# Performance work log

Measured on AMD Instinct MI355X. Metric: run time of the kernel, lower is better.

Reference implementation:

```python
import jax, jax.numpy as jnp
import numpy as np


def setup_inputs() -> dict:
    key = jax.random.key(0)
    k1, k2, k3, k4 = jax.random.split(key, 4)
    B, S, K, N = 4, 2048, 4096, 4096
    # int8-valued quantized activations / weights (held in int32 containers)
    a = jax.random.randint(k1, (B, S, K), -128, 128, dtype=jnp.int32)
    w = jax.random.randint(k2, (K, N), -128, 128, dtype=jnp.int32)
    # per-token activation scale and per-output-column weight scale
    a_scale = jax.random.uniform(k3, (B, S, 1), dtype=jnp.float32) * 0.01
    w_scale = jax.random.uniform(k4, (1, N), dtype=jnp.float32) * 0.01
    return {"a": a, "a_scale": a_scale, "w": w, "w_scale": w_scale}


def reference(a, a_scale, w, w_scale):
    # int8 GEMM with int32 accumulation (torch._int_mm equivalent),
    # batched over B instead of a per-slice Python loop.
    acc = jnp.einsum("bsk,kn->bsn", a, w)  # int32 accumulate
    # dequant epilogue: out = acc * (a_scale * w_scale), then cast to model dtype
    out = acc.astype(jnp.float32) * (a_scale * w_scale)  # [B,S,N]
    return out.astype(jnp.float32)
```

## Files before the change

### kernel.cpp

```cpp
#include <hip/hip_runtime.h>


#define M_TOT 8192
#define N_TOT 4096
#define K_TOT 4096
#define NT_K  (K_TOT / 64)
#define TILE_BYTES 16384

typedef int v4i  __attribute__((ext_vector_type(4)));
typedef int v16i __attribute__((ext_vector_type(16)));

typedef const __attribute__((address_space(1))) unsigned char* gas1_t;
typedef __attribute__((address_space(3))) unsigned char* las3_t;

__device__ __forceinline__ int pack4(int4 v) {
    return (int)((unsigned)(v.x & 255) | ((unsigned)(v.y & 255) << 8) |
                 ((unsigned)(v.z & 255) << 16) | ((unsigned)v.w << 24));
}

__global__ __launch_bounds__(256) void pack_a_kernel(const int* __restrict__ a,
                                                     unsigned char* __restrict__ a8) {
    __shared__ int4 stage[128 * 16];
    const int b = blockIdx.x;
    const int kt = b & (NT_K - 1);
    const int m128 = b >> 6;
    const int mt = m128 >> 1;
    const int mhalf = m128 & 1;
    const int t = threadIdx.x;
#pragma unroll
    for (int i = 0; i < 8; ++i) {
        const int idx16 = i * 256 + t;
        const int r = idx16 >> 4;
        const int c = idx16 & 15;
        int4 v = *(const int4*)(a + (size_t)(mt * 256 + mhalf * 128 + r) * K_TOT +
                                kt * 64 + c * 4);
        stage[r * 16 + (c ^ (r & 15))] = v;
    }
    __syncthreads();
    unsigned char* outp = a8 + (size_t)(mt * NT_K + kt) * TILE_BYTES;
#pragma unroll
    for (int q = 0; q < 2; ++q) {
        const int id = q * 256 + t;
        const int j = id >> 7;
        const int r = id & 127;
        int4 d0 = stage[r * 16 + ((j * 4 + 0) ^ (r & 15))];
        int4 d1 = stage[r * 16 + ((j * 4 + 1) ^ (r & 15))];
        int4 d2 = stage[r * 16 + ((j * 4 + 2) ^ (r & 15))];
        int4 d3 = stage[r * 16 + ((j * 4 + 3) ^ (r & 15))];
        int4 p = { pack4(d0), pack4(d1), pack4(d2), pack4(d3) };
        *(int4*)(outp + j * 4096 + (mhalf * 128 + r) * 16) = p;
    }
}

__global__ __launch_bounds__(256) void pack_w_kernel(const int* __restrict__ w,
                                                     unsigned char* __restrict__ w8) {
    __shared__ int stage[64 * 128];
    const int b = blockIdx.x;
    const int kt = b & (NT_K - 1);
    const int n128 = b >> 6;
    const int nt = n128 >> 1;
    const int nhalf = n128 & 1;
    const int t = threadIdx.x;
#pragma unroll
    for (int i = 0; i < 8; ++i) {
        const int idx = i * 256 + t;
        const int k = idx >> 5;
        const int c4 = idx & 31;
        int4 v = *(const int4*)(w + (size_t)(kt * 64 + k) * N_TOT +
                                nt * 256 + nhalf * 128 + c4 * 4);
        *(int4*)&stage[k * 128 + c4 * 4] = v;
    }
    __syncthreads();
    unsigned char* outp = w8 + (size_t)(nt * NT_K + kt) * TILE_BYTES;
#pragma unroll
    for (int q = 0; q < 2; ++q) {
        const int id = q * 256 + t;
        const int j = id >> 7;
        const int n = id & 127;
        int4 p;
#pragma unroll
        for (int qq = 0; qq < 4; ++qq) {
            int4 bb;
            bb.x = stage[(j * 16 + qq * 4 + 0) * 128 + n];
            bb.y = stage[(j * 16 + qq * 4 + 1) * 128 + n];
            bb.z = stage[(j * 16 + qq * 4 + 2) * 128 + n];
            bb.w = stage[(j * 16 + qq * 4 + 3) * 128 + n];
            ((int*)&p)[qq] = pack4(bb);
        }
        *(int4*)(outp + j * 4096 + (nhalf * 128 + n) * 16) = p;
    }
}

__global__ __launch_bounds__(512, 2) void gemm_i8_kernel(
    const unsigned char* __restrict__ a8, const unsigned char* __restrict__ w8,
    const float* __restrict__ a_scale, const float* __restrict__ w_scale,
    float* __restrict__ out) {

    __shared__ __attribute__((aligned(16))) unsigned char sm[4][2][TILE_BYTES];

    const int t = threadIdx.x;
    const int lane = t & 63;
    const int wid = t >> 6;
    const int wr = wid >> 2;
    const int wc = wid & 3;
    const int hi = lane >> 5;
    const int lo32 = lane & 31;

    int bid = blockIdx.x;
    bid = (bid & 7) * (512 / 8) + (bid >> 3);
    const int mt = bid >> 4;
    const int nt = bid & 15;

    const unsigned char* a_tiles = a8 + (size_t)mt * NT_K * TILE_BYTES;
    const unsigned char* w_tiles = w8 + (size_t)nt * NT_K * TILE_BYTES;

    v16i acc[4][2] = {};

#define STAGE_TILE(bN, gaP, gbP) do {                                             \
    __builtin_amdgcn_global_load_lds((gas1_t)((gaP) + t * 16),                    \
        (las3_t)&sm[bN][0][t * 16], 16, 0, 0);                                    \
    __builtin_amdgcn_global_load_lds((gas1_t)((gaP) + 8192 + t * 16),             \
        (las3_t)&sm[bN][0][8192 + t * 16], 16, 0, 0);                             \
    __builtin_amdgcn_global_load_lds((gas1_t)((gbP) + t * 16),                    \
        (las3_t)&sm[bN][1][t * 16], 16, 0, 0);                                    \
    __builtin_amdgcn_global_load_lds((gas1_t)((gbP) + 8192 + t * 16),             \
        (las3_t)&sm[bN][1][8192 + t * 16], 16, 0, 0);                             \
} while (0)

#define ITER(b0, b3, Tcur) do {                                                   \
    const int Tp = ((Tcur) + 3 <= NT_K - 1) ? (Tcur) + 3 : NT_K - 1;              \
    STAGE_TILE(b3, a_tiles + (size_t)Tp * TILE_BYTES,                             \
                   w_tiles + (size_t)Tp * TILE_BYTES);                            \
    const unsigned char* lA = &sm[b0][0][0];                                      \
    const unsigned char* lB = &sm[b0][1][0];                                      \
    v4i af0[4], bf0[2], af1[4], bf1[2];                                           \
    _Pragma("unroll")                                                             \
    for (int mi = 0; mi < 4; ++mi)                                                \
        af0[mi] = *(const v4i*)(lA + hi * 4096 + (wr * 128 + mi * 32 + lo32) * 16);\
    _Pragma("unroll")                                                             \
    for (int ni = 0; ni < 2; ++ni)                                                \
        bf0[ni] = *(const v4i*)(lB + hi * 4096 + (wc * 64 + ni * 32 + lo32) * 16);\
    __builtin_amdgcn_sched_barrier(0);   \
    _Pragma("unroll")                                                             \
    for (int mi = 0; mi < 4; ++mi)                                                \
        af1[mi] = *(const v4i*)(lA + (2 + hi) * 4096 + (wr * 128 + mi * 32 + lo32) * 16);\
    _Pragma("unroll")                                                             \
    for (int ni = 0; ni < 2; ++ni)                                                \
        bf1[ni] = *(const v4i*)(lB + (2 + hi) * 4096 + (wc * 64 + ni * 32 + lo32) * 16);\
    asm volatile("s_waitcnt vmcnt(8)" ::: "memory");                              \
    __builtin_amdgcn_s_barrier();                                                 \
    asm volatile("s_waitcnt lgkmcnt(6)" ::: "memory");                            \
    __builtin_amdgcn_sched_barrier(0);                                            \
    __builtin_amdgcn_s_setprio(1);                                                \
    _Pragma("unroll")                                                             \
    for (int mi = 0; mi < 4; ++mi)                                                \
        _Pragma("unroll")                                                         \
        for (int ni = 0; ni < 2; ++ni)                                            \
            acc[mi][ni] = __builtin_amdgcn_mfma_i32_32x32x32_i8(                  \
                af0[mi], bf0[ni], acc[mi][ni], 0, 0, 0);                          \
    asm volatile("s_waitcnt lgkmcnt(0)" ::: "memory");                            \
    __builtin_amdgcn_sched_barrier(0);                                            \
    _Pragma("unroll")                                                             \
    for (int mi = 0; mi < 4; ++mi)                                                \
        _Pragma("unroll")                                                         \
        for (int ni = 0; ni < 2; ++ni)                                            \
            acc[mi][ni] = __builtin_amdgcn_mfma_i32_32x32x32_i8(                  \
                af1[mi], bf1[ni], acc[mi][ni], 0, 0, 0);                          \
    __builtin_amdgcn_s_setprio(0);                                                \
    __builtin_amdgcn_s_barrier();                                                 \
} while (0)

    STAGE_TILE(0, a_tiles, w_tiles);
    STAGE_TILE(1, a_tiles + TILE_BYTES, w_tiles + TILE_BYTES);
    STAGE_TILE(2, a_tiles + 2 * TILE_BYTES, w_tiles + 2 * TILE_BYTES);
    asm volatile("s_waitcnt vmcnt(8)" ::: "memory");
    __builtin_amdgcn_s_barrier();

    int T = 0;
#pragma unroll 1
    for (int u = 0; u < 16; ++u) {
        ITER(0, 3, T);
        ITER(1, 0, T + 1);
        ITER(2, 1, T + 2);
        ITER(3, 2, T + 3);
        T += 4;
    }

    asm volatile("s_waitcnt vmcnt(0)" ::: "memory");

#undef STAGE_TILE
#undef ITER

    __syncthreads();
    float* scA = (float*)&sm[0][0][0];
    float* scW = scA + 256;
    if (t < 256) scA[t] = a_scale[mt * 256 + t];
    else         scW[t - 256] = w_scale[nt * 256 + (t - 256)];
    __syncthreads();

    const int row0 = mt * 256 + wr * 128;
    const int col0 = nt * 256 + wc * 64;
#pragma unroll
    for (int mi = 0; mi < 4; ++mi) {
#pragma unroll
        for (int r = 0; r < 16; ++r) {
            const int rloc = wr * 128 + mi * 32 + (r & 3) + 8 * (r >> 2) + 4 * hi;
            const float as = scA[rloc];
            float* orow = out + (size_t)(row0 - wr * 128 + rloc) * N_TOT + col0 + lo32;
#pragma unroll
            for (int ni = 0; ni < 2; ++ni)
                orow[ni * 32] = (float)acc[mi][ni][r] * as * scW[wc * 64 + ni * 32 + lo32];
        }
    }
    (void)row0;
}

extern "C" void kernel_launch(void* const* d_in, const int* in_sizes, int n_in,
                              void* d_out, int out_size, void* d_ws, size_t ws_size,
                              hipStream_t stream) {
    const int*   a       = (const int*)d_in[0];
    const float* a_scale = (const float*)d_in[1];
    const int*   w       = (const int*)d_in[2];
    const float* w_scale = (const float*)d_in[3];
    float*       out     = (float*)d_out;

    unsigned char* a8 = (unsigned char*)d_ws;
    unsigned char* w8 = a8 + (size_t)M_TOT * K_TOT;

    pack_a_kernel<<<(M_TOT / 128) * NT_K, 256, 0, stream>>>(a, a8);
    pack_w_kernel<<<(N_TOT / 128) * NT_K, 256, 0, stream>>>(w, w8);
    gemm_i8_kernel<<<(M_TOT / 256) * (N_TOT / 256), 512, 0, stream>>>(
        a8, w8, a_scale, w_scale, out);
}
```

Before: 397.0 us.

## Double-buffer LDS fragments in registers to overlap reads with MFMAs

Restructures the main K loop so each iteration issues the LDS fragment reads for the next K tile into a second register set, then runs the MFMAs on fragments loaded in the previous iteration. This replaces the old pattern of reading both K halves and waiting on lgkmcnt before each MFMA group. The aim is to hide LDS read latency behind matrix-core work. The cost is roughly 48 more VGPRs for the second fragment set, which could create register pressure, plus a prologue read of the first tile. It also simplifies the epilogue row-address calculation.

```diff
diff --git a/kernel.cpp b/kernel.cpp
--- a/kernel.cpp
+++ b/kernel.cpp
@@ -116,6 +116,9 @@
 
     v16i acc[4][2] = {};
 
+    v4i afA0[4], afA1[4], bfA0[2], bfA1[2];
+    v4i afB0[4], afB1[4], bfB0[2], bfB1[2];
+
 #define STAGE_TILE(bN, gaP, gbP) do {                                             \
     __builtin_amdgcn_global_load_lds((gas1_t)((gaP) + t * 16),                    \
         (las3_t)&sm[bN][0][t * 16], 16, 0, 0);                                    \
@@ -127,45 +130,46 @@
         (las3_t)&sm[bN][1][8192 + t * 16], 16, 0, 0);                             \
 } while (0)
 
-#define ITER(b0, b3, Tcur) do {                                                   \
-    const int Tp = ((Tcur) + 3 <= NT_K - 1) ? (Tcur) + 3 : NT_K - 1;              \
-    STAGE_TILE(b3, a_tiles + (size_t)Tp * TILE_BYTES,                             \
-                   w_tiles + (size_t)Tp * TILE_BYTES);                            \
-    const unsigned char* lA = &sm[b0][0][0];                                      \
-    const unsigned char* lB = &sm[b0][1][0];                                      \
-    v4i af0[4], bf0[2], af1[4], bf1[2];                                           \
-    _Pragma("unroll")                                                             \
-    for (int mi = 0; mi < 4; ++mi)                                                \
-        af0[mi] = *(const v4i*)(lA + hi * 4096 + (wr * 128 + mi * 32 + lo32) * 16);\
-    _Pragma("unroll")                                                             \
-    for (int ni = 0; ni < 2; ++ni)                                                \
-        bf0[ni] = *(const v4i*)(lB + hi * 4096 + (wc * 64 + ni * 32 + lo32) * 16);\
-    __builtin_amdgcn_sched_barrier(0);   \
-    _Pragma("unroll")                                                             \
-    for (int mi = 0; mi < 4; ++mi)                                                \
-        af1[mi] = *(const v4i*)(lA + (2 + hi) * 4096 + (wr * 128 + mi * 32 + lo32) * 16);\
-    _Pragma("unroll")                                                             \
-    for (int ni = 0; ni < 2; ++ni)                                                \
-        bf1[ni] = *(const v4i*)(lB + (2 + hi) * 4096 + (wc * 64 + ni * 32 + lo32) * 16);\
-    asm volatile("s_waitcnt vmcnt(8)" ::: "memory");                              \
-    __builtin_amdgcn_s_barrier();                                                 \
-    asm volatile("s_waitcnt lgkmcnt(6)" ::: "memory");                            \
-    __builtin_amdgcn_sched_barrier(0);                                            \
-    __builtin_amdgcn_s_setprio(1);                                                \
+#define READ_FRAGS(P, bN) do {                                                    \
+    const unsigned char* lA_ = &sm[bN][0][hi * 4096 + (wr * 128 + lo32) * 16];    \
+    const unsigned char* lB_ = &sm[bN][1][hi * 4096 + (wc * 64 + lo32) * 16];     \
+    _Pragma("unroll")                                                             \
+    for (int mi = 0; mi < 4; ++mi) af##P##0[mi] = *(const v4i*)(lA_ + mi * 512);  \
+    _Pragma("unroll")                                                             \
+    for (int mi = 0; mi < 4; ++mi) af##P##1[mi] = *(const v4i*)(lA_ + 8192 + mi * 512);\
+    _Pragma("unroll")                                                             \
+    for (int ni = 0; ni < 2; ++ni) bf##P##0[ni] = *(const v4i*)(lB_ + ni * 512);  \
+    _Pragma("unroll")                                                             \
+    for (int ni = 0; ni < 2; ++ni) bf##P##1[ni] = *(const v4i*)(lB_ + 8192 + ni * 512);\
+} while (0)
+
+#define MFMA_ALL(P) do {                                                          \
     _Pragma("unroll")                                                             \
     for (int mi = 0; mi < 4; ++mi)                                                \
         _Pragma("unroll")                                                         \
         for (int ni = 0; ni < 2; ++ni)                                            \
             acc[mi][ni] = __builtin_amdgcn_mfma_i32_32x32x32_i8(                  \
-                af0[mi], bf0[ni], acc[mi][ni], 0, 0, 0);                          \
-    asm volatile("s_waitcnt lgkmcnt(0)" ::: "memory");                            \
-    __builtin_amdgcn_sched_barrier(0);                                            \
+                af##P##0[mi], bf##P##0[ni], acc[mi][ni], 0, 0, 0);                \
     _Pragma("unroll")                                                             \
     for (int mi = 0; mi < 4; ++mi)                                                \
         _Pragma("unroll")                                                         \
         for (int ni = 0; ni < 2; ++ni)                                            \
             acc[mi][ni] = __builtin_amdgcn_mfma_i32_32x32x32_i8(                  \
-                af1[mi], bf1[ni], acc[mi][ni], 0, 0, 0);                          \
+                af##P##1[mi], bf##P##1[ni], acc[mi][ni], 0, 0, 0);                \
+} while (0)
+
+#define ITER(Tcur, CUR, NXT, b1, b3) do {                                         \
+    const int Tp = ((Tcur) + 3 <= NT_K - 1) ? (Tcur) + 3 : NT_K - 1;              \
+    STAGE_TILE(b3, a_tiles + (size_t)Tp * TILE_BYTES,                             \
+                   w_tiles + (size_t)Tp * TILE_BYTES);                            \
+    asm volatile("s_waitcnt vmcnt(8)" ::: "memory");                              \
+    __builtin_amdgcn_s_barrier();                                                 \
+    asm volatile("s_waitcnt lgkmcnt(0)" ::: "memory");                            \
+    __builtin_amdgcn_sched_barrier(0);                                            \
+    __builtin_amdgcn_s_setprio(1);                                                \
+    READ_FRAGS(NXT, b1);                                                          \
+    __builtin_amdgcn_sched_barrier(0);   \
+    MFMA_ALL(CUR);                                                                \
     __builtin_amdgcn_s_setprio(0);                                                \
     __builtin_amdgcn_s_barrier();                                                 \
 } while (0)
@@ -175,20 +179,23 @@
     STAGE_TILE(2, a_tiles + 2 * TILE_BYTES, w_tiles + 2 * TILE_BYTES);
     asm volatile("s_waitcnt vmcnt(8)" ::: "memory");
     __builtin_amdgcn_s_barrier();
+    READ_FRAGS(A, 0);
 
     int T = 0;
 #pragma unroll 1
     for (int u = 0; u < 16; ++u) {
-        ITER(0, 3, T);
-        ITER(1, 0, T + 1);
-        ITER(2, 1, T + 2);
-        ITER(3, 2, T + 3);
+        ITER(T,     A, B, 1, 3);
+        ITER(T + 1, B, A, 2, 0);
+        ITER(T + 2, A, B, 3, 1);
+        ITER(T + 3, B, A, 0, 2);
         T += 4;
     }
 
     asm volatile("s_waitcnt vmcnt(0)" ::: "memory");
 
 #undef STAGE_TILE
+#undef READ_FRAGS
+#undef MFMA_ALL
 #undef ITER
 
     __syncthreads();
@@ -198,7 +205,6 @@
     else         scW[t - 256] = w_scale[nt * 256 + (t - 256)];
     __syncthreads();
 
-    const int row0 = mt * 256 + wr * 128;
     const int col0 = nt * 256 + wc * 64;
 #pragma unroll
     for (int mi = 0; mi < 4; ++mi) {
@@ -206,13 +212,12 @@
         for (int r = 0; r < 16; ++r) {
             const int rloc = wr * 128 + mi * 32 + (r & 3) + 8 * (r >> 2) + 4 * hi;
             const float as = scA[rloc];
-            float* orow = out + (size_t)(row0 - wr * 128 + rloc) * N_TOT + col0 + lo32;
+            float* orow = out + (size_t)(mt * 256 + rloc) * N_TOT + col0 + lo32;
 #pragma unroll
             for (int ni = 0; ni < 2; ++ni)
                 orow[ni * 32] = (float)acc[mi][ni][r] * as * scW[wc * 64 + ni * 32 + lo32];
         }
     }
-    (void)row0;
 }
 
 extern "C" void kernel_launch(void* const* d_in, const int* in_sizes, int n_in,
```

After: 400.0 us. No clear change (+0.8%).
